# Optimization experiments

Measured on AMD Instinct MI355X. Metric: run time of the kernel, lower is better.

## Reference

```python
import jax, jax.numpy as jnp
import numpy as np

NUM_NODES = 100000
NODE_DIM = 64
MEM_DIM = 64
EMBED = 64   # out_channels
HEADS = 2
IN_DIM = NODE_DIM + MEM_DIM  # 128
N = 50000    # batch nodes (len(n_id))
E = 800000   # edges in local subgraph


def setup_inputs() -> dict:
    key = jax.random.key(0)
    ks = jax.random.split(key, 12)
    s = 1.0 / np.sqrt(IN_DIM)
    inp = {
        "n_id": jax.random.randint(ks[0], (N,), 0, NUM_NODES),
        "edge_index": jax.random.randint(ks[1], (2, E), 0, N),
        # non-learned TGN memory state (detached in forward)
        "memory_table": jax.random.normal(ks[2], (NUM_NODES, MEM_DIM), jnp.float32),
        # learned node embedding table
        "emb_table": jax.random.normal(ks[3], (NUM_NODES, NODE_DIM), jnp.float32),
        # TransformerConv linear layers; weights stored [in, out] so y = x @ W + b
        "Wq": jax.random.normal(ks[4], (IN_DIM, HEADS * EMBED), jnp.float32) * s,
        "bq": jnp.zeros((HEADS * EMBED,), jnp.float32),
        "Wk": jax.random.normal(ks[5], (IN_DIM, HEADS * EMBED), jnp.float32) * s,
        "bk": jnp.zeros((HEADS * EMBED,), jnp.float32),
        "Wv": jax.random.normal(ks[6], (IN_DIM, HEADS * EMBED), jnp.float32) * s,
        "bv": jnp.zeros((HEADS * EMBED,), jnp.float32),
        "Wskip": jax.random.normal(ks[7], (IN_DIM, EMBED), jnp.float32) * s,
        "bskip": jnp.zeros((EMBED,), jnp.float32),
    }
    return inp


def reference(n_id, edge_index, memory_table, emb_table, Wq, bq, Wk, bk, Wv, bv, Wskip, bskip):
    # memory lookup (detached) + embedding lookup + concat([emb, mem])
    z = jax.lax.stop_gradient(memory_table[n_id])          # [N, MEM_DIM]
    x = jnp.concatenate([emb_table[n_id], z], axis=-1)     # [N, IN_DIM]

    q = (x @ Wq + bq).reshape(N, HEADS, EMBED)
    k = (x @ Wk + bk).reshape(N, HEADS, EMBED)
    v = (x @ Wv + bv).reshape(N, HEADS, EMBED)

    src, dst = edge_index[0], edge_index[1]
    # per-edge attention score: (q_i . k_j) / sqrt(d), i = dst, j = src
    score = jnp.einsum("ehd,ehd->eh", q[dst], k[src]) / np.sqrt(EMBED)  # [E, H]
    # scatter-softmax over incoming edges of each destination node
    smax = jax.ops.segment_max(score, dst, num_segments=N)              # [N, H]
    exps = jnp.exp(score - smax[dst])                                   # [E, H]
    denom = jax.ops.segment_sum(exps, dst, num_segments=N)              # [N, H]
    alpha = exps / denom[dst]                                           # [E, H]

    msg = alpha[:, :, None] * v[src]                                    # [E, H, D]
    out = jax.ops.segment_sum(msg, dst, num_segments=N)                 # [N, H, D]
    out = out.mean(axis=1)                                              # concat=False -> mean over heads
    out = out + x @ Wskip + bskip                                       # root_weight skip
    return out
```

## Files before the change

### kernel.cpp

```cpp
#include <hip/hip_runtime.h>
#include <math.h>


typedef unsigned int uint32;
typedef unsigned short ushort16;
typedef __attribute__((ext_vector_type(8))) short short8;
typedef __attribute__((ext_vector_type(4))) float floatx4;

__device__ __forceinline__ ushort16 f2bf(float f) {
  union { float f; uint32 u; } x; x.f = f;
  uint32 r = x.u + 0x7fffu + ((x.u >> 16) & 1u);
  return (ushort16)(r >> 16);
}
__device__ __forceinline__ float bf_lo(uint32 u) {
  union { uint32 u; float f; } x; x.u = u << 16; return x.f;
}
__device__ __forceinline__ float bf_hi(uint32 u) {
  union { uint32 u; float f; } x; x.u = u & 0xffff0000u; return x.f;
}

__global__ __launch_bounds__(256) void prep_w_kernel(
    const float* __restrict__ Wq, const float* __restrict__ bq,
    const float* __restrict__ Wk, const float* __restrict__ bk,
    const float* __restrict__ Wv, const float* __restrict__ bv,
    const float* __restrict__ Ws, const float* __restrict__ bs,
    ushort16* __restrict__ Wt, float* __restrict__ ball) {
  int idx = blockIdx.x * 256 + threadIdx.x;
  if (idx < 448 * 128) {
    int n = idx >> 7, k = idx & 127;
    float w;
    if (n < 128)      w = Wq[k * 128 + n];
    else if (n < 256) w = Wk[k * 128 + (n - 128)];
    else if (n < 384) w = Wv[k * 128 + (n - 256)];
    else              w = Ws[k * 64 + (n - 384)];
    Wt[idx] = f2bf(w);
  }
  if (idx < 448) {
    float b;
    if (idx < 128)      b = bq[idx];
    else if (idx < 256) b = bk[idx - 128];
    else if (idx < 384) b = bv[idx - 256];
    else                b = bs[idx - 384];
    ball[idx] = b;
  }
}

__global__ __launch_bounds__(256) void gather_hist_kernel(
    const int* __restrict__ n_id, const float* __restrict__ memtab,
    const float* __restrict__ embtab, ushort16* __restrict__ xb, int N,
    const int* __restrict__ dstA, int E, int* __restrict__ counts) {
  int idx = blockIdx.x * blockDim.x + threadIdx.x;
  if (idx < N * 32) {
    int node = idx >> 5;
    int c4 = (idx & 31) * 4;
    int srcrow = n_id[node];
    float4 val;
    if (c4 < 64)
      val = *(const float4*)(embtab + (size_t)srcrow * 64 + c4);
    else
      val = *(const float4*)(memtab + (size_t)srcrow * 64 + (c4 - 64));
    uint2 p;
    p.x = (uint32)f2bf(val.x) | ((uint32)f2bf(val.y) << 16);
    p.y = (uint32)f2bf(val.z) | ((uint32)f2bf(val.w) << 16);
    *(uint2*)(xb + (size_t)node * 128 + c4) = p;
  }
  if (idx < E) atomicAdd(&counts[dstA[idx]], 1);
}

__global__ __launch_bounds__(256) void scan1_kernel(const int* __restrict__ counts,
                                                    int* __restrict__ offs,
                                                    int* __restrict__ bsum, int N) {
  __shared__ int s[256];
  int b = blockIdx.x, t = threadIdx.x;
  int base = b * 4096 + t * 16;
  int vals[16];
  int sum = 0;
#pragma unroll
  for (int i = 0; i < 16; ++i) {
    int idx = base + i;
    vals[i] = (idx < N) ? counts[idx] : 0;
    sum += vals[i];
  }
  s[t] = sum;
  __syncthreads();
  for (int off = 1; off < 256; off <<= 1) {
    int vv = (t >= off) ? s[t - off] : 0;
    __syncthreads();
    s[t] += vv;
    __syncthreads();
  }
  int run = (t > 0) ? s[t - 1] : 0;
#pragma unroll
  for (int i = 0; i < 16; ++i) {
    int idx = base + i;
    if (idx < N) offs[idx] = run;
    run += vals[i];
  }
  if (t == 255) bsum[b] = s[255];
}

__global__ __launch_bounds__(256) void scan3_kernel(int* __restrict__ offs,
                                                    const int* __restrict__ bsum,
                                                    int N, int E) {
  int i = blockIdx.x * blockDim.x + threadIdx.x;
  if (i < N) {
    int blk = i >> 12;
    int add = 0;
    for (int j = 0; j < blk; ++j) add += bsum[j];
    offs[i] += add;
  }
  if (i == 0) offs[N] = E;
}

__global__ __launch_bounds__(256) void scatter_kernel(
    const int* __restrict__ srcA, const int* __restrict__ dstA, int E,
    const int* __restrict__ offs, int* __restrict__ cursor,
    int* __restrict__ sorted_src) {
  int e = blockIdx.x * blockDim.x + threadIdx.x;
  if (e < E) {
    int d = dstA[e];
    int p = offs[d] + atomicAdd(&cursor[d], 1);
    sorted_src[p] = srcA[e];
  }
}

#define LDA 136
__global__ __launch_bounds__(256) void qkv_mfma_kernel(
    const ushort16* __restrict__ xb, const ushort16* __restrict__ Wt,
    const float* __restrict__ ball,
    ushort16* __restrict__ qb, ushort16* __restrict__ kb, ushort16* __restrict__ vb,
    float* __restrict__ outskip, int N) {
  __shared__ ushort16 As[128 * LDA];
  __shared__ ushort16 Bs[64 * LDA];
  int t = threadIdx.x;
  int row0 = blockIdx.x * 128;
  int col0 = blockIdx.y * 64;

#pragma unroll
  for (int rep = 0; rep < 8; ++rep) {
    int idx = rep * 256 + t;
    int r = idx >> 4, c = idx & 15;
    uint4 val = make_uint4(0u, 0u, 0u, 0u);
    int grow = row0 + r;
    if (grow < N) val = *(const uint4*)(xb + (size_t)grow * 128 + c * 8);
    *(uint4*)&As[r * LDA + c * 8] = val;
  }
#pragma unroll
  for (int rep = 0; rep < 4; ++rep) {
    int idx = rep * 256 + t;
    int r = idx >> 4, c = idx & 15;
    uint4 val = *(const uint4*)(Wt + (size_t)(col0 + r) * 128 + c * 8);
    *(uint4*)&Bs[r * LDA + c * 8] = val;
  }
  __syncthreads();

  int wave = t >> 6, lane = t & 63;
  int m_base = wave * 32;
  int lrow = lane & 15, quad = lane >> 4;

  floatx4 acc[2][4];
#pragma unroll
  for (int i = 0; i < 2; ++i)
#pragma unroll
    for (int j = 0; j < 4; ++j) acc[i][j] = (floatx4)(0.f);

#pragma unroll
  for (int kk = 0; kk < 4; ++kk) {
    int koff = kk * 32 + quad * 8;
    short8 a0 = *(const short8*)&As[(m_base + lrow) * LDA + koff];
    short8 a1 = *(const short8*)&As[(m_base + 16 + lrow) * LDA + koff];
    short8 b0 = *(const short8*)&Bs[(lrow) * LDA + koff];
    short8 b1 = *(const short8*)&Bs[(16 + lrow) * LDA + koff];
    short8 b2 = *(const short8*)&Bs[(32 + lrow) * LDA + koff];
    short8 b3 = *(const short8*)&Bs[(48 + lrow) * LDA + koff];
    acc[0][0] = __builtin_amdgcn_mfma_f32_16x16x32_bf16(a0, b0, acc[0][0], 0, 0, 0);
    acc[0][1] = __builtin_amdgcn_mfma_f32_16x16x32_bf16(a0, b1, acc[0][1], 0, 0, 0);
    acc[0][2] = __builtin_amdgcn_mfma_f32_16x16x32_bf16(a0, b2, acc[0][2], 0, 0, 0);
    acc[0][3] = __builtin_amdgcn_mfma_f32_16x16x32_bf16(a0, b3, acc[0][3], 0, 0, 0);
    acc[1][0] = __builtin_amdgcn_mfma_f32_16x16x32_bf16(a1, b0, acc[1][0], 0, 0, 0);
    acc[1][1] = __builtin_amdgcn_mfma_f32_16x16x32_bf16(a1, b1, acc[1][1], 0, 0, 0);
    acc[1][2] = __builtin_amdgcn_mfma_f32_16x16x32_bf16(a1, b2, acc[1][2], 0, 0, 0);
    acc[1][3] = __builtin_amdgcn_mfma_f32_16x16x32_bf16(a1, b3, acc[1][3], 0, 0, 0);
  }

  int dest = blockIdx.y;
#pragma unroll
  for (int ct = 0; ct < 4; ++ct) {
    int gcol = col0 + ct * 16 + lrow;
    float bias = ball[gcol];
#pragma unroll
    for (int rt = 0; rt < 2; ++rt) {
#pragma unroll
      for (int r = 0; r < 4; ++r) {
        int grow = row0 + m_base + rt * 16 + quad * 4 + r;
        if (grow >= N) continue;
        float o = acc[rt][ct][r] + bias;
        if (dest < 2)      qb[(size_t)grow * 128 + gcol]         = f2bf(o);
        else if (dest < 4) kb[(size_t)grow * 128 + (gcol - 128)] = f2bf(o);
        else if (dest < 6) vb[(size_t)grow * 128 + (gcol - 256)] = f2bf(o);
        else               outskip[(size_t)grow * 64 + (gcol - 384)] = o;
      }
    }
  }
}

#define EXPC 0.1803368801111244f
__global__ __launch_bounds__(256) void attn_kernel(
    const ushort16* __restrict__ qb, const ushort16* __restrict__ kb,
    const ushort16* __restrict__ vb, const int* __restrict__ offs,
    const int* __restrict__ ssrc, float* __restrict__ out, int N) {
  int tid = threadIdx.x;
  int wave = tid >> 6, lane = tid & 63;
  int half = lane >> 5;
  int node = (blockIdx.x * 4 + wave) * 2 + half;
  int l32 = lane & 31;
  int head = l32 >> 4;
  int l16 = lane & 15;
  bool valid = node < N;

  int e0 = 0, e1 = 0;
  if (valid) { e0 = offs[node]; e1 = offs[node + 1]; }
  int hoff = head * 64 + 4 * l16;

  float qx = 0.f, qy = 0.f, qz = 0.f, qw = 0.f;
  if (valid) {
    uint2 qu = *(const uint2*)(qb + (size_t)node * 128 + hoff);
    qx = bf_lo(qu.x); qy = bf_hi(qu.x); qz = bf_lo(qu.y); qw = bf_hi(qu.y);
  }

  float l = 0.f, a0 = 0.f, a1 = 0.f, a2 = 0.f, a3 = 0.f;

  uint2 kA = make_uint2(0, 0), vA = make_uint2(0, 0);
  uint2 kB = make_uint2(0, 0), vB = make_uint2(0, 0);
  if (e0 < e1) {
    int s = ssrc[e0];
    kA = *(const uint2*)(kb + (size_t)s * 128 + hoff);
    vA = *(const uint2*)(vb + (size_t)s * 128 + hoff);
  }
  if (e0 + 1 < e1) {
    int s = ssrc[e0 + 1];
    kB = *(const uint2*)(kb + (size_t)s * 128 + hoff);
    vB = *(const uint2*)(vb + (size_t)s * 128 + hoff);
  }

  for (int e = e0; e < e1; e += 2) {
    uint2 k0 = kA, v0 = vA, k1 = kB, v1 = vB;
    bool h1 = (e + 1 < e1);
    int en = e + 2;
    if (en < e1) {
      int s = ssrc[en];
      kA = *(const uint2*)(kb + (size_t)s * 128 + hoff);
      vA = *(const uint2*)(vb + (size_t)s * 128 + hoff);
    }
    if (en + 1 < e1) {
      int s = ssrc[en + 1];
      kB = *(const uint2*)(kb + (size_t)s * 128 + hoff);
      vB = *(const uint2*)(vb + (size_t)s * 128 + hoff);
    }

    float p0 = qx * bf_lo(k0.x);
    p0 = fmaf(qy, bf_hi(k0.x), p0);
    p0 = fmaf(qz, bf_lo(k0.y), p0);
    p0 = fmaf(qw, bf_hi(k0.y), p0);
    float p1 = qx * bf_lo(k1.x);
    p1 = fmaf(qy, bf_hi(k1.x), p1);
    p1 = fmaf(qz, bf_lo(k1.y), p1);
    p1 = fmaf(qw, bf_hi(k1.y), p1);
#pragma unroll
    for (int o = 1; o < 16; o <<= 1) {
      p0 += __shfl_xor(p0, o);
      p1 += __shfl_xor(p1, o);
    }
    float w0 = exp2f(p0 * EXPC);
    float w1 = h1 ? exp2f(p1 * EXPC) : 0.f;
    l += w0 + w1;
    a0 = fmaf(w0, bf_lo(v0.x), a0);
    a1 = fmaf(w0, bf_hi(v0.x), a1);
    a2 = fmaf(w0, bf_lo(v0.y), a2);
    a3 = fmaf(w0, bf_hi(v0.y), a3);
    a0 = fmaf(w1, bf_lo(v1.x), a0);
    a1 = fmaf(w1, bf_hi(v1.x), a1);
    a2 = fmaf(w1, bf_lo(v1.y), a2);
    a3 = fmaf(w1, bf_hi(v1.y), a3);
  }

  float inv = (l > 0.f) ? 0.5f / l : 0.f;
  float r0 = a0 * inv, r1 = a1 * inv, r2 = a2 * inv, r3 = a3 * inv;
  r0 += __shfl_xor(r0, 16);
  r1 += __shfl_xor(r1, 16);
  r2 += __shfl_xor(r2, 16);
  r3 += __shfl_xor(r3, 16);
  if (valid && head == 0) {
    float* op = out + (size_t)node * 64 + 4 * l16;
    float4 cur = *(float4*)op;
    cur.x += r0; cur.y += r1; cur.z += r2; cur.w += r3;
    *(float4*)op = cur;
  }
}

extern "C" void kernel_launch(void* const* d_in, const int* in_sizes, int n_in,
                              void* d_out, int out_size, void* d_ws, size_t ws_size,
                              hipStream_t stream) {
  const int* n_id = (const int*)d_in[0];
  const int* eidx = (const int*)d_in[1];
  const float* memtab = (const float*)d_in[2];
  const float* embtab = (const float*)d_in[3];
  const float* Wq = (const float*)d_in[4];
  const float* bq = (const float*)d_in[5];
  const float* Wk = (const float*)d_in[6];
  const float* bk = (const float*)d_in[7];
  const float* Wv = (const float*)d_in[8];
  const float* bv = (const float*)d_in[9];
  const float* Wskip = (const float*)d_in[10];
  const float* bskip = (const float*)d_in[11];

  int N = in_sizes[0];
  int E = in_sizes[1] / 2;
  const int* srcA = eidx;
  const int* dstA = eidx + E;
  float* out = (float*)d_out;

  char* w = (char*)d_ws;
  ushort16* xb = (ushort16*)w; w += (size_t)N * 128 * 2;
  ushort16* qb = (ushort16*)w; w += (size_t)N * 128 * 2;
  ushort16* kb = (ushort16*)w; w += (size_t)N * 128 * 2;
  ushort16* vb = (ushort16*)w; w += (size_t)N * 128 * 2;
  ushort16* Wt = (ushort16*)w; w += (size_t)448 * 128 * 2;
  float* ball = (float*)w;     w += (size_t)448 * 4;
  int* counts = (int*)w;       w += (size_t)N * 4;
  int* cursor = (int*)w;       w += (size_t)N * 4;
  int* offs = (int*)w;         w += (size_t)(N + 1) * 4;
  int* bsum = (int*)w;         w += (size_t)1024 * 4;
  int* ssrc = (int*)w;         w += (size_t)E * 4;

  hipMemsetAsync(counts, 0, (size_t)2 * N * 4, stream);

  prep_w_kernel<<<(448 * 128 + 255) / 256, 256, 0, stream>>>(
      Wq, bq, Wk, bk, Wv, bv, Wskip, bskip, Wt, ball);

  int gh_threads = (N * 32 > E) ? N * 32 : E;
  gather_hist_kernel<<<(gh_threads + 255) / 256, 256, 0, stream>>>(
      n_id, memtab, embtab, xb, N, dstA, E, counts);

  int NB = (N + 4095) / 4096;
  scan1_kernel<<<NB, 256, 0, stream>>>(counts, offs, bsum, N);
  scan3_kernel<<<(N + 255) / 256, 256, 0, stream>>>(offs, bsum, N, E);

  scatter_kernel<<<(E + 255) / 256, 256, 0, stream>>>(srcA, dstA, E, offs, cursor, ssrc);

  dim3 ggrid((N + 127) / 128, 7);
  qkv_mfma_kernel<<<ggrid, 256, 0, stream>>>(xb, Wt, ball, qb, kb, vb, out, N);

  attn_kernel<<<(N + 7) / 8, 256, 0, stream>>>(qb, kb, vb, offs, ssrc, out, N);
}
```

Before: 307.9 us.

## Fuse gather into QKV GEMM, single-block scan, 4 nodes per wave in attention

The node-feature gather and bf16 conversion move into the QKV MFMA kernel, so the intermediate x buffer is no longer written and re-read. Each block now loops over all seven weight column tiles while keeping its A fragments in registers. The two-kernel scan becomes one single-block 1024-thread scan, and the weight prep is merged with the degree histogram. The attention kernel now handles four nodes per wave with 8-element vector loads, iterating to the maximum degree within the wave. This cuts launches and memory traffic but serialises the scan onto one block and may waste lanes on degree imbalance.

```diff
diff --git a/kernel.cpp b/kernel.cpp
--- a/kernel.cpp
+++ b/kernel.cpp
@@ -18,13 +18,26 @@
 __device__ __forceinline__ float bf_hi(uint32 u) {
   union { uint32 u; float f; } x; x.u = u & 0xffff0000u; return x.f;
 }
-
-__global__ __launch_bounds__(256) void prep_w_kernel(
+__device__ __forceinline__ void unpack8(uint4 u, float* f) {
+  f[0] = bf_lo(u.x); f[1] = bf_hi(u.x); f[2] = bf_lo(u.y); f[3] = bf_hi(u.y);
+  f[4] = bf_lo(u.z); f[5] = bf_hi(u.z); f[6] = bf_lo(u.w); f[7] = bf_hi(u.w);
+}
+__device__ __forceinline__ uint4 pack8(float4 a, float4 b) {
+  uint4 r;
+  r.x = (uint32)f2bf(a.x) | ((uint32)f2bf(a.y) << 16);
+  r.y = (uint32)f2bf(a.z) | ((uint32)f2bf(a.w) << 16);
+  r.z = (uint32)f2bf(b.x) | ((uint32)f2bf(b.y) << 16);
+  r.w = (uint32)f2bf(b.z) | ((uint32)f2bf(b.w) << 16);
+  return r;
+}
+
+__global__ __launch_bounds__(256) void prep_hist_kernel(
     const float* __restrict__ Wq, const float* __restrict__ bq,
     const float* __restrict__ Wk, const float* __restrict__ bk,
     const float* __restrict__ Wv, const float* __restrict__ bv,
     const float* __restrict__ Ws, const float* __restrict__ bs,
-    ushort16* __restrict__ Wt, float* __restrict__ ball) {
+    ushort16* __restrict__ Wt, float* __restrict__ ball,
+    const int* __restrict__ dstA, int E, int* __restrict__ counts) {
   int idx = blockIdx.x * 256 + threadIdx.x;
   if (idx < 448 * 128) {
     int n = idx >> 7, k = idx & 127;
@@ -43,73 +56,39 @@
     else                b = bs[idx - 384];
     ball[idx] = b;
   }
-}
-
-__global__ __launch_bounds__(256) void gather_hist_kernel(
-    const int* __restrict__ n_id, const float* __restrict__ memtab,
-    const float* __restrict__ embtab, ushort16* __restrict__ xb, int N,
-    const int* __restrict__ dstA, int E, int* __restrict__ counts) {
-  int idx = blockIdx.x * blockDim.x + threadIdx.x;
-  if (idx < N * 32) {
-    int node = idx >> 5;
-    int c4 = (idx & 31) * 4;
-    int srcrow = n_id[node];
-    float4 val;
-    if (c4 < 64)
-      val = *(const float4*)(embtab + (size_t)srcrow * 64 + c4);
-    else
-      val = *(const float4*)(memtab + (size_t)srcrow * 64 + (c4 - 64));
-    uint2 p;
-    p.x = (uint32)f2bf(val.x) | ((uint32)f2bf(val.y) << 16);
-    p.y = (uint32)f2bf(val.z) | ((uint32)f2bf(val.w) << 16);
-    *(uint2*)(xb + (size_t)node * 128 + c4) = p;
-  }
   if (idx < E) atomicAdd(&counts[dstA[idx]], 1);
 }
 
-__global__ __launch_bounds__(256) void scan1_kernel(const int* __restrict__ counts,
-                                                    int* __restrict__ offs,
-                                                    int* __restrict__ bsum, int N) {
-  __shared__ int s[256];
-  int b = blockIdx.x, t = threadIdx.x;
-  int base = b * 4096 + t * 16;
-  int vals[16];
-  int sum = 0;
-#pragma unroll
-  for (int i = 0; i < 16; ++i) {
-    int idx = base + i;
-    vals[i] = (idx < N) ? counts[idx] : 0;
-    sum += vals[i];
-  }
-  s[t] = sum;
-  __syncthreads();
-  for (int off = 1; off < 256; off <<= 1) {
-    int vv = (t >= off) ? s[t - off] : 0;
+__global__ __launch_bounds__(1024) void scan_kernel(
+    const int* __restrict__ counts, int* __restrict__ offs, int N, int E) {
+  __shared__ int ws[16];
+  int t = threadIdx.x;
+  int lane = t & 63, wave = t >> 6;
+  int running = 0;
+  int nIter = (N + 1023) >> 10;
+  for (int it = 0; it < nIter; ++it) {
+    int idx = (it << 10) + t;
+    int v = (idx < N) ? counts[idx] : 0;
+    int p = v;
+#pragma unroll
+    for (int o = 1; o < 64; o <<= 1) {
+      int u = __shfl_up(p, o);
+      if (lane >= o) p += u;
+    }
+    if (lane == 63) ws[wave] = p;
     __syncthreads();
-    s[t] += vv;
+    int wpre = 0, tot = 0;
+#pragma unroll
+    for (int w = 0; w < 16; ++w) {
+      int s = ws[w];
+      if (w < wave) wpre += s;
+      tot += s;
+    }
+    if (idx < N) offs[idx] = running + wpre + (p - v);
+    running += tot;
     __syncthreads();
   }
-  int run = (t > 0) ? s[t - 1] : 0;
-#pragma unroll
-  for (int i = 0; i < 16; ++i) {
-    int idx = base + i;
-    if (idx < N) offs[idx] = run;
-    run += vals[i];
-  }
-  if (t == 255) bsum[b] = s[255];
-}
-
-__global__ __launch_bounds__(256) void scan3_kernel(int* __restrict__ offs,
-                                                    const int* __restrict__ bsum,
-                                                    int N, int E) {
-  int i = blockIdx.x * blockDim.x + threadIdx.x;
-  if (i < N) {
-    int blk = i >> 12;
-    int add = 0;
-    for (int j = 0; j < blk; ++j) add += bsum[j];
-    offs[i] += add;
-  }
-  if (i == 0) offs[N] = E;
+  if (t == 0) offs[N] = E;
 }
 
 __global__ __launch_bounds__(256) void scatter_kernel(
@@ -126,31 +105,31 @@
 
 #define LDA 136
 __global__ __launch_bounds__(256) void qkv_mfma_kernel(
-    const ushort16* __restrict__ xb, const ushort16* __restrict__ Wt,
-    const float* __restrict__ ball,
+    const int* __restrict__ n_id, const float* __restrict__ embtab,
+    const float* __restrict__ memtab,
+    const ushort16* __restrict__ Wt, const float* __restrict__ ball,
     ushort16* __restrict__ qb, ushort16* __restrict__ kb, ushort16* __restrict__ vb,
     float* __restrict__ outskip, int N) {
   __shared__ ushort16 As[128 * LDA];
   __shared__ ushort16 Bs[64 * LDA];
   int t = threadIdx.x;
   int row0 = blockIdx.x * 128;
-  int col0 = blockIdx.y * 64;
 
 #pragma unroll
   for (int rep = 0; rep < 8; ++rep) {
     int idx = rep * 256 + t;
     int r = idx >> 4, c = idx & 15;
-    uint4 val = make_uint4(0u, 0u, 0u, 0u);
     int grow = row0 + r;
-    if (grow < N) val = *(const uint4*)(xb + (size_t)grow * 128 + c * 8);
-    *(uint4*)&As[r * LDA + c * 8] = val;
-  }
-#pragma unroll
-  for (int rep = 0; rep < 4; ++rep) {
-    int idx = rep * 256 + t;
-    int r = idx >> 4, c = idx & 15;
-    uint4 val = *(const uint4*)(Wt + (size_t)(col0 + r) * 128 + c * 8);
-    *(uint4*)&Bs[r * LDA + c * 8] = val;
+    uint4 outv = make_uint4(0u, 0u, 0u, 0u);
+    if (grow < N) {
+      int srcrow = n_id[grow];
+      const float* srcp = (c < 8) ? (embtab + (size_t)srcrow * 64 + c * 8)
+                                  : (memtab + (size_t)srcrow * 64 + (c - 8) * 8);
+      float4 f0 = *(const float4*)srcp;
+      float4 f1 = *(const float4*)(srcp + 4);
+      outv = pack8(f0, f1);
+    }
+    *(uint4*)&As[r * LDA + c * 8] = outv;
   }
   __syncthreads();
 
@@ -158,49 +137,67 @@
   int m_base = wave * 32;
   int lrow = lane & 15, quad = lane >> 4;
 
-  floatx4 acc[2][4];
-#pragma unroll
-  for (int i = 0; i < 2; ++i)
-#pragma unroll
-    for (int j = 0; j < 4; ++j) acc[i][j] = (floatx4)(0.f);
-
+  short8 af0[4], af1[4];
 #pragma unroll
   for (int kk = 0; kk < 4; ++kk) {
     int koff = kk * 32 + quad * 8;
-    short8 a0 = *(const short8*)&As[(m_base + lrow) * LDA + koff];
-    short8 a1 = *(const short8*)&As[(m_base + 16 + lrow) * LDA + koff];
-    short8 b0 = *(const short8*)&Bs[(lrow) * LDA + koff];
-    short8 b1 = *(const short8*)&Bs[(16 + lrow) * LDA + koff];
-    short8 b2 = *(const short8*)&Bs[(32 + lrow) * LDA + koff];
-    short8 b3 = *(const short8*)&Bs[(48 + lrow) * LDA + koff];
-    acc[0][0] = __builtin_amdgcn_mfma_f32_16x16x32_bf16(a0, b0, acc[0][0], 0, 0, 0);
-    acc[0][1] = __builtin_amdgcn_mfma_f32_16x16x32_bf16(a0, b1, acc[0][1], 0, 0, 0);
-    acc[0][2] = __builtin_amdgcn_mfma_f32_16x16x32_bf16(a0, b2, acc[0][2], 0, 0, 0);
-    acc[0][3] = __builtin_amdgcn_mfma_f32_16x16x32_bf16(a0, b3, acc[0][3], 0, 0, 0);
-    acc[1][0] = __builtin_amdgcn_mfma_f32_16x16x32_bf16(a1, b0, acc[1][0], 0, 0, 0);
-    acc[1][1] = __builtin_amdgcn_mfma_f32_16x16x32_bf16(a1, b1, acc[1][1], 0, 0, 0);
-    acc[1][2] = __builtin_amdgcn_mfma_f32_16x16x32_bf16(a1, b2, acc[1][2], 0, 0, 0);
-    acc[1][3] = __builtin_amdgcn_mfma_f32_16x16x32_bf16(a1, b3, acc[1][3], 0, 0, 0);
-  }
-
-  int dest = blockIdx.y;
-#pragma unroll
-  for (int ct = 0; ct < 4; ++ct) {
-    int gcol = col0 + ct * 16 + lrow;
-    float bias = ball[gcol];
-#pragma unroll
-    for (int rt = 0; rt < 2; ++rt) {
-#pragma unroll
-      for (int r = 0; r < 4; ++r) {
-        int grow = row0 + m_base + rt * 16 + quad * 4 + r;
-        if (grow >= N) continue;
-        float o = acc[rt][ct][r] + bias;
-        if (dest < 2)      qb[(size_t)grow * 128 + gcol]         = f2bf(o);
-        else if (dest < 4) kb[(size_t)grow * 128 + (gcol - 128)] = f2bf(o);
-        else if (dest < 6) vb[(size_t)grow * 128 + (gcol - 256)] = f2bf(o);
-        else               outskip[(size_t)grow * 64 + (gcol - 384)] = o;
+    af0[kk] = *(const short8*)&As[(m_base + lrow) * LDA + koff];
+    af1[kk] = *(const short8*)&As[(m_base + 16 + lrow) * LDA + koff];
+  }
+
+  for (int ct = 0; ct < 7; ++ct) {
+    int col0 = ct * 64;
+#pragma unroll
+    for (int rep = 0; rep < 4; ++rep) {
+      int idx = rep * 256 + t;
+      int r = idx >> 4, c = idx & 15;
+      uint4 val = *(const uint4*)(Wt + (size_t)(col0 + r) * 128 + c * 8);
+      *(uint4*)&Bs[r * LDA + c * 8] = val;
+    }
+    __syncthreads();
+
+    floatx4 acc[2][4];
+#pragma unroll
+    for (int i = 0; i < 2; ++i)
+#pragma unroll
+      for (int j = 0; j < 4; ++j) acc[i][j] = (floatx4)(0.f);
+
+#pragma unroll
+    for (int kk = 0; kk < 4; ++kk) {
+      int koff = kk * 32 + quad * 8;
+      short8 b0 = *(const short8*)&Bs[(lrow) * LDA + koff];
+      short8 b1 = *(const short8*)&Bs[(16 + lrow) * LDA + koff];
+      short8 b2 = *(const short8*)&Bs[(32 + lrow) * LDA + koff];
+      short8 b3 = *(const short8*)&Bs[(48 + lrow) * LDA + koff];
+      acc[0][0] = __builtin_amdgcn_mfma_f32_16x16x32_bf16(af0[kk], b0, acc[0][0], 0, 0, 0);
+      acc[0][1] = __builtin_amdgcn_mfma_f32_16x16x32_bf16(af0[kk], b1, acc[0][1], 0, 0, 0);
+      acc[0][2] = __builtin_amdgcn_mfma_f32_16x16x32_bf16(af0[kk], b2, acc[0][2], 0, 0, 0);
+      acc[0][3] = __builtin_amdgcn_mfma_f32_16x16x32_bf16(af0[kk], b3, acc[0][3], 0, 0, 0);
+      acc[1][0] = __builtin_amdgcn_mfma_f32_16x16x32_bf16(af1[kk], b0, acc[1][0], 0, 0, 0);
+      acc[1][1] = __builtin_amdgcn_mfma_f32_16x16x32_bf16(af1[kk], b1, acc[1][1], 0, 0, 0);
+      acc[1][2] = __builtin_amdgcn_mfma_f32_16x16x32_bf16(af1[kk], b2, acc[1][2], 0, 0, 0);
+      acc[1][3] = __builtin_amdgcn_mfma_f32_16x16x32_bf16(af1[kk], b3, acc[1][3], 0, 0, 0);
+    }
+
+#pragma unroll
+    for (int jt = 0; jt < 4; ++jt) {
+      int gcol = col0 + jt * 16 + lrow;
+      float bias = ball[gcol];
+#pragma unroll
+      for (int rt = 0; rt < 2; ++rt) {
+#pragma unroll
+        for (int r = 0; r < 4; ++r) {
+          int grow = row0 + m_base + rt * 16 + quad * 4 + r;
+          if (grow >= N) continue;
+          float o = acc[rt][jt][r] + bias;
+          if (ct < 2)      qb[(size_t)grow * 128 + gcol]         = f2bf(o);
+          else if (ct < 4) kb[(size_t)grow * 128 + (gcol - 128)] = f2bf(o);
+          else if (ct < 6) vb[(size_t)grow * 128 + (gcol - 256)] = f2bf(o);
+          else             outskip[(size_t)grow * 64 + (gcol - 384)] = o;
+        }
       }
     }
+    __syncthreads();
   }
 }
 
@@ -211,90 +208,86 @@
     const int* __restrict__ ssrc, float* __restrict__ out, int N) {
   int tid = threadIdx.x;
   int wave = tid >> 6, lane = tid & 63;
-  int half = lane >> 5;
-  int node = (blockIdx.x * 4 + wave) * 2 + half;
-  int l32 = lane & 31;
-  int head = l32 >> 4;
+  int nsub = lane >> 4;
   int l16 = lane & 15;
+  int head = l16 >> 3;
+  int l8 = lane & 7;
+  int node = (blockIdx.x * 4 + wave) * 4 + nsub;
   bool valid = node < N;
+  int nodeC = valid ? node : 0;
 
   int e0 = 0, e1 = 0;
   if (valid) { e0 = offs[node]; e1 = offs[node + 1]; }
-  int hoff = head * 64 + 4 * l16;
-
-  float qx = 0.f, qy = 0.f, qz = 0.f, qw = 0.f;
-  if (valid) {
-    uint2 qu = *(const uint2*)(qb + (size_t)node * 128 + hoff);
-    qx = bf_lo(qu.x); qy = bf_hi(qu.x); qz = bf_lo(qu.y); qw = bf_hi(qu.y);
-  }
-
-  float l = 0.f, a0 = 0.f, a1 = 0.f, a2 = 0.f, a3 = 0.f;
-
-  uint2 kA = make_uint2(0, 0), vA = make_uint2(0, 0);
-  uint2 kB = make_uint2(0, 0), vB = make_uint2(0, 0);
-  if (e0 < e1) {
-    int s = ssrc[e0];
-    kA = *(const uint2*)(kb + (size_t)s * 128 + hoff);
-    vA = *(const uint2*)(vb + (size_t)s * 128 + hoff);
-  }
-  if (e0 + 1 < e1) {
-    int s = ssrc[e0 + 1];
-    kB = *(const uint2*)(kb + (size_t)s * 128 + hoff);
-    vB = *(const uint2*)(vb + (size_t)s * 128 + hoff);
-  }
-
-  for (int e = e0; e < e1; e += 2) {
-    uint2 k0 = kA, v0 = vA, k1 = kB, v1 = vB;
-    bool h1 = (e + 1 < e1);
-    int en = e + 2;
-    if (en < e1) {
-      int s = ssrc[en];
-      kA = *(const uint2*)(kb + (size_t)s * 128 + hoff);
-      vA = *(const uint2*)(vb + (size_t)s * 128 + hoff);
-    }
-    if (en + 1 < e1) {
-      int s = ssrc[en + 1];
-      kB = *(const uint2*)(kb + (size_t)s * 128 + hoff);
-      vB = *(const uint2*)(vb + (size_t)s * 128 + hoff);
-    }
-
-    float p0 = qx * bf_lo(k0.x);
-    p0 = fmaf(qy, bf_hi(k0.x), p0);
-    p0 = fmaf(qz, bf_lo(k0.y), p0);
-    p0 = fmaf(qw, bf_hi(k0.y), p0);
-    float p1 = qx * bf_lo(k1.x);
-    p1 = fmaf(qy, bf_hi(k1.x), p1);
-    p1 = fmaf(qz, bf_lo(k1.y), p1);
-    p1 = fmaf(qw, bf_hi(k1.y), p1);
-#pragma unroll
-    for (int o = 1; o < 16; o <<= 1) {
-      p0 += __shfl_xor(p0, o);
-      p1 += __shfl_xor(p1, o);
-    }
-    float w0 = exp2f(p0 * EXPC);
-    float w1 = h1 ? exp2f(p1 * EXPC) : 0.f;
-    l += w0 + w1;
-    a0 = fmaf(w0, bf_lo(v0.x), a0);
-    a1 = fmaf(w0, bf_hi(v0.x), a1);
-    a2 = fmaf(w0, bf_lo(v0.y), a2);
-    a3 = fmaf(w0, bf_hi(v0.y), a3);
-    a0 = fmaf(w1, bf_lo(v1.x), a0);
-    a1 = fmaf(w1, bf_hi(v1.x), a1);
-    a2 = fmaf(w1, bf_lo(v1.y), a2);
-    a3 = fmaf(w1, bf_hi(v1.y), a3);
+  int deg = e1 - e0;
+  int md = deg;
+  md = max(md, __shfl_xor(md, 16));
+  md = max(md, __shfl_xor(md, 32));
+
+  int hoff = head * 64 + l8 * 8;
+  float qf[8];
+  {
+    uint4 qu = *(const uint4*)(qb + (size_t)nodeC * 128 + hoff);
+    unpack8(qu, qf);
+  }
+
+  float l = 0.f;
+  float a[8];
+#pragma unroll
+  for (int j = 0; j < 8; ++j) a[j] = 0.f;
+
+  uint4 k0v = make_uint4(0, 0, 0, 0), v0v = k0v, k1v = k0v, v1v = k0v;
+  if (md > 0) {
+    int e = e0;
+    int s = (e < e1) ? ssrc[e] : 0;
+    k0v = *(const uint4*)(kb + (size_t)s * 128 + hoff);
+    v0v = *(const uint4*)(vb + (size_t)s * 128 + hoff);
+  }
+  if (md > 1) {
+    int e = e0 + 1;
+    int s = (e < e1) ? ssrc[e] : 0;
+    k1v = *(const uint4*)(kb + (size_t)s * 128 + hoff);
+    v1v = *(const uint4*)(vb + (size_t)s * 128 + hoff);
+  }
+
+  for (int i = 0; i < md; ++i) {
+    uint4 kc = k0v, vc = v0v;
+    k0v = k1v; v0v = v1v;
+    if (i + 2 < md) {
+      int e = e0 + i + 2;
+      int s = (e < e1) ? ssrc[e] : 0;
+      k1v = *(const uint4*)(kb + (size_t)s * 128 + hoff);
+      v1v = *(const uint4*)(vb + (size_t)s * 128 + hoff);
+    }
+    float kf[8], vf[8];
+    unpack8(kc, kf);
+    unpack8(vc, vf);
+    float p = qf[0] * kf[0];
+#pragma unroll
+    for (int j = 1; j < 8; ++j) p = fmaf(qf[j], kf[j], p);
+    p += __shfl_xor(p, 1);
+    p += __shfl_xor(p, 2);
+    p += __shfl_xor(p, 4);
+    float w = (i < deg) ? exp2f(p * EXPC) : 0.f;
+    l += w;
+#pragma unroll
+    for (int j = 0; j < 8; ++j) a[j] = fmaf(w, vf[j], a[j]);
   }
 
   float inv = (l > 0.f) ? 0.5f / l : 0.f;
-  float r0 = a0 * inv, r1 = a1 * inv, r2 = a2 * inv, r3 = a3 * inv;
-  r0 += __shfl_xor(r0, 16);
-  r1 += __shfl_xor(r1, 16);
-  r2 += __shfl_xor(r2, 16);
-  r3 += __shfl_xor(r3, 16);
+  float r[8];
+#pragma unroll
+  for (int j = 0; j < 8; ++j) r[j] = a[j] * inv;
+#pragma unroll
+  for (int j = 0; j < 8; ++j) r[j] += __shfl_xor(r[j], 8);
+
   if (valid && head == 0) {
-    float* op = out + (size_t)node * 64 + 4 * l16;
-    float4 cur = *(float4*)op;
-    cur.x += r0; cur.y += r1; cur.z += r2; cur.w += r3;
-    *(float4*)op = cur;
+    float* op = out + (size_t)node * 64 + l8 * 8;
+    float4 c0 = *(float4*)op;
+    float4 c1 = *(float4*)(op + 4);
+    c0.x += r[0]; c0.y += r[1]; c0.z += r[2]; c0.w += r[3];
+    c1.x += r[4]; c1.y += r[5]; c1.z += r[6]; c1.w += r[7];
+    *(float4*)op = c0;
+    *(float4*)(op + 4) = c1;
   }
 }
 
@@ -321,7 +314,6 @@
   float* out = (float*)d_out;
 
   char* w = (char*)d_ws;
-  ushort16* xb = (ushort16*)w; w += (size_t)N * 128 * 2;
   ushort16* qb = (ushort16*)w; w += (size_t)N * 128 * 2;
   ushort16* kb = (ushort16*)w; w += (size_t)N * 128 * 2;
   ushort16* vb = (ushort16*)w; w += (size_t)N * 128 * 2;
@@ -330,26 +322,20 @@
   int* counts = (int*)w;       w += (size_t)N * 4;
   int* cursor = (int*)w;       w += (size_t)N * 4;
   int* offs = (int*)w;         w += (size_t)(N + 1) * 4;
-  int* bsum = (int*)w;         w += (size_t)1024 * 4;
   int* ssrc = (int*)w;         w += (size_t)E * 4;
 
   hipMemsetAsync(counts, 0, (size_t)2 * N * 4, stream);
 
-  prep_w_kernel<<<(448 * 128 + 255) / 256, 256, 0, stream>>>(
-      Wq, bq, Wk, bk, Wv, bv, Wskip, bskip, Wt, ball);
-
-  int gh_threads = (N * 32 > E) ? N * 32 : E;
-  gather_hist_kernel<<<(gh_threads + 255) / 256, 256, 0, stream>>>(
-      n_id, memtab, embtab, xb, N, dstA, E, counts);
-
-  int NB = (N + 4095) / 4096;
-  scan1_kernel<<<NB, 256, 0, stream>>>(counts, offs, bsum, N);
-  scan3_kernel<<<(N + 255) / 256, 256, 0, stream>>>(offs, bsum, N, E);
+  int k1_threads = (448 * 128 > E) ? 448 * 128 : E;
+  prep_hist_kernel<<<(k1_threads + 255) / 256, 256, 0, stream>>>(
+      Wq, bq, Wk, bk, Wv, bv, Wskip, bskip, Wt, ball, dstA, E, counts);
+
+  scan_kernel<<<1, 1024, 0, stream>>>(counts, offs, N, E);
 
   scatter_kernel<<<(E + 255) / 256, 256, 0, stream>>>(srcA, dstA, E, offs, cursor, ssrc);
 
-  dim3 ggrid((N + 127) / 128, 7);
-  qkv_mfma_kernel<<<ggrid, 256, 0, stream>>>(xb, Wt, ball, qb, kb, vb, out, N);
-
-  attn_kernel<<<(N + 7) / 8, 256, 0, stream>>>(qb, kb, vb, offs, ssrc, out, N);
-}
+  qkv_mfma_kernel<<<(N + 127) / 128, 256, 0, stream>>>(
+      n_id, embtab, memtab, Wt, ball, qb, kb, vb, out, N);
+
+  attn_kernel<<<(N + 15) / 16, 256, 0, stream>>>(qb, kb, vb, offs, ssrc, out, N);
+}
```

Measured after the change: 339.4 us. 10.2% more time.
